# Performance work log

Measured on AMD Instinct MI355X. Metric: run time of the kernel, lower is better.

The kernel has to match this reference:

```python
import jax, jax.numpy as jnp
import numpy as np

B, L, H, E = 4, 2048, 8, 64
S, D = L, E  # causal mask forces L == S


def setup_inputs() -> dict:
    key = jax.random.key(0)
    kq, kk, kv, km = jax.random.split(key, 4)
    return {
        "queries": jax.random.normal(kq, (B, L, H, E), dtype=jnp.float32),
        "keys": jax.random.normal(kk, (B, S, H, E), dtype=jnp.float32),
        "values": jax.random.normal(kv, (B, S, H, D), dtype=jnp.float32),
        "map": jax.random.normal(km, (S, S), dtype=jnp.float32),
    }


def reference(queries, keys, values, map):
    # queries: [B,L,H,E], keys: [B,S,H,E], values: [B,S,H,D], map: [S,S]
    E_ = queries.shape[-1]
    scale = 1.0 / jnp.sqrt(jnp.asarray(E_, dtype=queries.dtype))
    # raw attention scores: [B,H,L,S]
    scores = jnp.einsum("blhe,bshe->bhls", queries, keys)
    # mix scores with learned map along the key axis: [B,H,L,S]
    scores = jnp.einsum("bhls,st->bhlt", scores, map)
    # causal mask (TriangularCausalMask: triu with diagonal=1 is masked)
    Lq = queries.shape[1]
    causal = jnp.triu(jnp.ones((Lq, Lq), dtype=bool), k=1)  # [L,S]
    scores = jnp.where(causal[None, None, :, :], -jnp.inf, scores)
    attn = jax.nn.softmax(scale * scores, axis=-1)  # dropout p=0.0 -> identity
    out = jnp.einsum("bhls,bshd->blhd", attn, values)  # [B,L,H,D]
    return out
```

## Files before the change

kernel.cpp:

```cpp
#include <hip/hip_runtime.h>


typedef short bf16x8 __attribute__((ext_vector_type(8)));
typedef float f32x4 __attribute__((ext_vector_type(4)));
typedef float f32x16 __attribute__((ext_vector_type(16)));
typedef unsigned short u16x8 __attribute__((ext_vector_type(8)));

typedef __attribute__((address_space(1))) const void gvoid;
typedef __attribute__((address_space(3))) void lvoid;

__device__ __forceinline__ unsigned short f2bf(float x) {
  unsigned int u = __float_as_uint(x);
  u += 0x7FFFu + ((u >> 16) & 1u);
  return (unsigned short)(u >> 16);
}
__device__ __forceinline__ float bf2f(unsigned short h) {
  return __uint_as_float(((unsigned int)h) << 16);
}

__device__ __forceinline__ void gload16(const unsigned short* g, unsigned short* l) {
  __builtin_amdgcn_global_load_lds((gvoid*)g, (lvoid*)l, 16, 0, 0);
}

__device__ __forceinline__ void stage_tile(const unsigned short* __restrict__ g,
                                           int gstride, unsigned short* l,
                                           int rows, int tid) {
  const int lane = tid & 63, w = tid >> 6;
  const int nch = rows << 3;
  for (int c0 = (w << 6); c0 < nch; c0 += 256) {
    const int c = c0 + lane;
    const int row = c >> 3;
    const int bir = (c & 7) << 4;
    const int sb = bir ^ ((row & 7) << 4);
    gload16(g + (size_t)row * gstride + (sb >> 1), l + (size_t)c0 * 8);
  }
}

__device__ __forceinline__ int swz(int row, int byteInRow) {
  return row * 128 + (byteInRow ^ ((row & 7) << 4));
}

__global__ __launch_bounds__(256) void prep_m(const float* __restrict__ M,
                                              unsigned short* __restrict__ Mh,
                                              unsigned short* __restrict__ Ml) {
  __shared__ float Ts[64][68];
  const int s0 = blockIdx.x << 6, t0 = blockIdx.y << 6;
  const int tid = threadIdx.x, r = tid >> 2, c0 = (tid & 3) << 4;
  const float* src = M + (size_t)(s0 + r) * 2048 + t0 + c0;
#pragma unroll
  for (int j = 0; j < 4; ++j)
    *(float4*)&Ts[r][c0 + 4 * j] = *(const float4*)(src + 4 * j);
  __syncthreads();
  u16x8 h0, h1, l0v, l1v;
#pragma unroll
  for (int j = 0; j < 8; ++j) {
    float x = Ts[c0 + j][r];
    unsigned short hh = f2bf(x);
    h0[j] = hh; l0v[j] = f2bf(x - bf2f(hh));
  }
#pragma unroll
  for (int j = 8; j < 16; ++j) {
    float x = Ts[c0 + j][r];
    unsigned short hh = f2bf(x);
    h1[j - 8] = hh; l1v[j - 8] = f2bf(x - bf2f(hh));
  }
  const size_t o = (size_t)(t0 + r) * 2048 + s0 + c0;
  *(u16x8*)(Mh + o) = h0; *(u16x8*)(Mh + o + 8) = h1;
  *(u16x8*)(Ml + o) = l0v; *(u16x8*)(Ml + o + 8) = l1v;
}

__global__ __launch_bounds__(256) void prep_kv(const float* __restrict__ src4d,
                                               unsigned short* __restrict__ Dh,
                                               unsigned short* __restrict__ Dl,
                                               int has_lo) {
  __shared__ float Ts[64][68];
  const int s0 = blockIdx.x << 6, bh = blockIdx.y;
  const int b = bh >> 3, h = bh & 7;
  const int tid = threadIdx.x, r = tid >> 2, c0 = (tid & 3) << 4;
  const float* src = src4d + ((size_t)(b * 2048 + s0 + r) * 8 + h) * 64 + c0;
#pragma unroll
  for (int j = 0; j < 4; ++j)
    *(float4*)&Ts[r][c0 + 4 * j] = *(const float4*)(src + 4 * j);
  __syncthreads();
  u16x8 h0, h1, l0v, l1v;
#pragma unroll
  for (int j = 0; j < 8; ++j) {
    float x = Ts[c0 + j][r];
    unsigned short hh = f2bf(x);
    h0[j] = hh; l0v[j] = f2bf(x - bf2f(hh));
  }
#pragma unroll
  for (int j = 8; j < 16; ++j) {
    float x = Ts[c0 + j][r];
    unsigned short hh = f2bf(x);
    h1[j - 8] = hh; l1v[j - 8] = f2bf(x - bf2f(hh));
  }
  const size_t o = ((size_t)bh * 64 + r) * 2048 + s0 + c0;
  *(u16x8*)(Dh + o) = h0; *(u16x8*)(Dh + o + 8) = h1;
  if (has_lo) { *(u16x8*)(Dl + o) = l0v; *(u16x8*)(Dl + o + 8) = l1v; }
}

__global__ __launch_bounds__(256) void km_mfma(
    const unsigned short* __restrict__ Mth, const unsigned short* __restrict__ Mtl,
    const unsigned short* __restrict__ Kth, const unsigned short* __restrict__ Ktl,
    unsigned short* __restrict__ KMh, unsigned short* __restrict__ KMl) {
  __shared__ __attribute__((aligned(16))) unsigned short sm[24576];
  unsigned short* MtH = sm;
  unsigned short* MtL = sm + 8192;
  unsigned short* KtH = sm + 16384;
  unsigned short* KtL = sm + 20480;
  const int tid = threadIdx.x, lane = tid & 63, w = tid >> 6;
  const int g = lane >> 4, li = lane & 15;
  const int t0 = blockIdx.x << 7;
  const int bh = blockIdx.y;
  const unsigned short* KtHb = Kth + (size_t)bh * 64 * 2048;
  const unsigned short* KtLb = Ktl + (size_t)bh * 64 * 2048;

  f32x4 acc[2][4];
#pragma unroll
  for (int mi = 0; mi < 2; ++mi)
#pragma unroll
    for (int ni = 0; ni < 4; ++ni) acc[mi][ni] = (f32x4){0.f, 0.f, 0.f, 0.f};

  for (int s0 = 0; s0 < 2048; s0 += 64) {
    __syncthreads();
    stage_tile(Mth + (size_t)t0 * 2048 + s0, 2048, MtH, 128, tid);
    stage_tile(Mtl + (size_t)t0 * 2048 + s0, 2048, MtL, 128, tid);
    stage_tile(KtHb + s0, 2048, KtH, 64, tid);
    stage_tile(KtLb + s0, 2048, KtL, 64, tid);
    asm volatile("s_waitcnt vmcnt(0)" ::: "memory");
    __syncthreads();
#pragma unroll
    for (int kk = 0; kk < 2; ++kk) {
      const int kb = (kk * 32 + 8 * g) * 2;
      bf16x8 aH[2], aL[2];
#pragma unroll
      for (int mi = 0; mi < 2; ++mi) {
        const int row = (w << 5) + (mi << 4) + li;
        aH[mi] = *(const bf16x8*)((const char*)MtH + swz(row, kb));
        aL[mi] = *(const bf16x8*)((const char*)MtL + swz(row, kb));
      }
#pragma unroll
      for (int ni = 0; ni < 4; ++ni) {
        const int row = (ni << 4) + li;
        const int off = swz(row, kb);
        const bf16x8 bH = *(const bf16x8*)((const char*)KtH + off);
        const bf16x8 bL = *(const bf16x8*)((const char*)KtL + off);
#pragma unroll
        for (int mi = 0; mi < 2; ++mi) {
          acc[mi][ni] = __builtin_amdgcn_mfma_f32_16x16x32_bf16(aH[mi], bH, acc[mi][ni], 0, 0, 0);
          acc[mi][ni] = __builtin_amdgcn_mfma_f32_16x16x32_bf16(aH[mi], bL, acc[mi][ni], 0, 0, 0);
          acc[mi][ni] = __builtin_amdgcn_mfma_f32_16x16x32_bf16(aL[mi], bH, acc[mi][ni], 0, 0, 0);
        }
      }
    }
  }
  const size_t base = (size_t)bh * 2048 * 64;
#pragma unroll
  for (int mi = 0; mi < 2; ++mi)
#pragma unroll
    for (int r = 0; r < 4; ++r) {
      const int trow = t0 + (w << 5) + (mi << 4) + (g << 2) + r;
#pragma unroll
      for (int ni = 0; ni < 4; ++ni) {
        const float x = acc[mi][ni][r];
        const unsigned short hh = f2bf(x);
        const size_t idx = base + (size_t)trow * 64 + (ni << 4) + li;
        KMh[idx] = hh;
        KMl[idx] = f2bf(x - bf2f(hh));
      }
    }
}

__global__ __launch_bounds__(256, 2) void attn32(
    const float* __restrict__ Q, const unsigned short* __restrict__ KMh,
    const unsigned short* __restrict__ KMl, const unsigned short* __restrict__ Vt,
    float* __restrict__ Out) {
  __shared__ __attribute__((aligned(16))) unsigned short sm[32768];
  const int tid = threadIdx.x, lane = tid & 63, w = tid >> 6;
  const int g2 = lane >> 5, li5 = lane & 31;
  unsigned short* PS = sm + 24576 + (w << 11);

  const int bid = (int)blockIdx.x;
  const int x = bid & 7;
  const int r = bid >> 3;
  const int m = r >> 2;
  const int bh = (x << 2) | (r & 3);
  const int lt = (m < 8) ? (15 - m) : (m - 8);
  const int b = bh >> 3, h = bh & 7;
  const int l0 = lt << 7;
  const int qg = l0 + (w << 5) + li5;

  bf16x8 qh[4], ql[4];
  {
    const float* qsrc = Q + (((size_t)(b * 2048 + qg) * 8 + h) << 6) + (g2 << 3);
#pragma unroll
    for (int kk = 0; kk < 4; ++kk) {
      const float4 v0 = *(const float4*)(qsrc + 16 * kk);
      const float4 v1 = *(const float4*)(qsrc + 16 * kk + 4);
      const float xs[8] = {v0.x, v0.y, v0.z, v0.w, v1.x, v1.y, v1.z, v1.w};
#pragma unroll
      for (int j = 0; j < 8; ++j) {
        const unsigned short hh = f2bf(xs[j]);
        qh[kk][j] = (short)hh;
        ql[kk][j] = (short)f2bf(xs[j] - bf2f(hh));
      }
    }
  }

  f32x16 o0 = {0,0,0,0,0,0,0,0,0,0,0,0,0,0,0,0};
  f32x16 o1 = {0,0,0,0,0,0,0,0,0,0,0,0,0,0,0,0};
  float m2 = -1e30f, lsum = 0.f;
  const float SC2 = 0.18033688011112042f;

  const unsigned short* KHb = KMh + (size_t)bh * 2048 * 64;
  const unsigned short* KLb = KMl + (size_t)bh * 2048 * 64;
  const unsigned short* VTb = Vt + (size_t)bh * 64 * 2048;

  const int jtmax_blk = 2 * lt + 1;
  const int jtmax_w = 2 * lt + (w >> 1);

  {
    unsigned short* s0b = sm;
    stage_tile(KHb, 64, s0b, 64, tid);
    stage_tile(KLb, 64, s0b + 4096, 64, tid);
    stage_tile(VTb, 2048, s0b + 8192, 64, tid);
  }
  asm volatile("s_waitcnt vmcnt(0)" ::: "memory");
  __builtin_amdgcn_s_barrier();
  __builtin_amdgcn_sched_barrier(0);

  for (int jt = 0; jt <= jtmax_blk; ++jt) {
    const int cur = jt & 1;
    if (jt < jtmax_blk) {
      unsigned short* nb = sm + (cur ^ 1) * 12288;
      stage_tile(KHb + (size_t)(jt + 1) * 4096, 64, nb, 64, tid);
      stage_tile(KLb + (size_t)(jt + 1) * 4096, 64, nb + 4096, 64, tid);
      stage_tile(VTb + (jt + 1) * 64, 2048, nb + 8192, 64, tid);
    }

    if (jt <= jtmax_w) {
      const unsigned short* KH = sm + cur * 12288;
      const unsigned short* KL = KH + 4096;
      const unsigned short* VT = KH + 8192;

      f32x16 z0 = {0,0,0,0,0,0,0,0,0,0,0,0,0,0,0,0};
      f32x16 z1 = {0,0,0,0,0,0,0,0,0,0,0,0,0,0,0,0};
      __builtin_amdgcn_s_setprio(1);
#pragma unroll
      for (int kk = 0; kk < 4; ++kk) {
        const int cb = 32 * kk + 16 * g2;
        const bf16x8 a0h = *(const bf16x8*)((const char*)KH + swz(li5, cb));
        const bf16x8 a0l = *(const bf16x8*)((const char*)KL + swz(li5, cb));
        const bf16x8 a1h = *(const bf16x8*)((const char*)KH + swz(32 + li5, cb));
        const bf16x8 a1l = *(const bf16x8*)((const char*)KL + swz(32 + li5, cb));
        z0 = __builtin_amdgcn_mfma_f32_32x32x16_bf16(a0h, qh[kk], z0, 0, 0, 0);
        z0 = __builtin_amdgcn_mfma_f32_32x32x16_bf16(a0h, ql[kk], z0, 0, 0, 0);
        z0 = __builtin_amdgcn_mfma_f32_32x32x16_bf16(a0l, qh[kk], z0, 0, 0, 0);
        z1 = __builtin_amdgcn_mfma_f32_32x32x16_bf16(a1h, qh[kk], z1, 0, 0, 0);
        z1 = __builtin_amdgcn_mfma_f32_32x32x16_bf16(a1h, ql[kk], z1, 0, 0, 0);
        z1 = __builtin_amdgcn_mfma_f32_32x32x16_bf16(a1l, qh[kk], z1, 0, 0, 0);
      }
      __builtin_amdgcn_s_setprio(0);

      const bool needmask = (jt * 64 + 63 > l0 + (w << 5));
      const int thr = qg - jt * 64;
      if (needmask) {
#pragma unroll
        for (int rr = 0; rr < 16; ++rr) {
          const int tl = (g2 << 2) + ((rr >> 2) << 3) + (rr & 3);
          z0[rr] = (tl > thr) ? -1e30f : z0[rr] * SC2;
          z1[rr] = (tl + 32 > thr) ? -1e30f : z1[rr] * SC2;
        }
      } else {
#pragma unroll
        for (int rr = 0; rr < 16; ++rr) { z0[rr] *= SC2; z1[rr] *= SC2; }
      }

      float t16[16];
#pragma unroll
      for (int rr = 0; rr < 16; ++rr) t16[rr] = fmaxf(z0[rr], z1[rr]);
#pragma unroll
      for (int s = 8; s; s >>= 1)
#pragma unroll
        for (int rr = 0; rr < 8; ++rr)
          if (rr < s) t16[rr] = fmaxf(t16[rr], t16[rr + s]);
      float mx = fmaxf(t16[0], __shfl_xor(t16[0], 32));
      const float m2n = fmaxf(m2, mx);
      const float fs = exp2f(m2 - m2n);
      m2 = m2n;
      float pv0[16], pv1[16];
#pragma unroll
      for (int rr = 0; rr < 16; ++rr) {
        pv0[rr] = exp2f(z0[rr] - m2n);
        pv1[rr] = exp2f(z1[rr] - m2n);
      }
      float s16[16];
#pragma unroll
      for (int rr = 0; rr < 16; ++rr) s16[rr] = pv0[rr] + pv1[rr];
#pragma unroll
      for (int s = 8; s; s >>= 1)
#pragma unroll
        for (int rr = 0; rr < 8; ++rr)
          if (rr < s) s16[rr] += s16[rr + s];
      float rs = s16[0] + __shfl_xor(s16[0], 32);
      lsum = lsum * fs + rs;
#pragma unroll
      for (int rr = 0; rr < 16; ++rr) { o0[rr] *= fs; o1[rr] *= fs; }

#pragma unroll
      for (int r2 = 0; r2 < 4; ++r2) {
        const int bb = (r2 << 4) + (g2 << 3);
        uint a0 = (uint)f2bf(pv0[4 * r2]) | ((uint)f2bf(pv0[4 * r2 + 1]) << 16);
        uint a1 = (uint)f2bf(pv0[4 * r2 + 2]) | ((uint)f2bf(pv0[4 * r2 + 3]) << 16);
        *(uint2*)((char*)PS + swz(li5, bb)) = make_uint2(a0, a1);
        uint b0 = (uint)f2bf(pv1[4 * r2]) | ((uint)f2bf(pv1[4 * r2 + 1]) << 16);
        uint b1 = (uint)f2bf(pv1[4 * r2 + 2]) | ((uint)f2bf(pv1[4 * r2 + 3]) << 16);
        *(uint2*)((char*)PS + swz(li5, 64 + bb)) = make_uint2(b0, b1);
      }

      __builtin_amdgcn_s_setprio(1);
#pragma unroll
      for (int kk = 0; kk < 4; ++kk) {
        const int cb = 32 * kk + 16 * g2;
        const bf16x8 pf = *(const bf16x8*)((const char*)PS + swz(li5, cb));
        const bf16x8 v0f = *(const bf16x8*)((const char*)VT + swz(li5, cb));
        const bf16x8 v1f = *(const bf16x8*)((const char*)VT + swz(32 + li5, cb));
        o0 = __builtin_amdgcn_mfma_f32_32x32x16_bf16(v0f, pf, o0, 0, 0, 0);
        o1 = __builtin_amdgcn_mfma_f32_32x32x16_bf16(v1f, pf, o1, 0, 0, 0);
      }
      __builtin_amdgcn_s_setprio(0);
    }

    asm volatile("s_waitcnt vmcnt(0)" ::: "memory");
    __builtin_amdgcn_s_barrier();
    __builtin_amdgcn_sched_barrier(0);
  }

  const float inv = 1.f / lsum;
  float* ob = Out + (((size_t)(b * 2048 + qg) * 8 + h) << 6);
#pragma unroll
  for (int r2 = 0; r2 < 4; ++r2) {
    const int doff = (g2 << 2) + (r2 << 3);
    float4 s0 = make_float4(o0[4 * r2] * inv, o0[4 * r2 + 1] * inv,
                            o0[4 * r2 + 2] * inv, o0[4 * r2 + 3] * inv);
    *(float4*)(ob + doff) = s0;
    float4 s1 = make_float4(o1[4 * r2] * inv, o1[4 * r2 + 1] * inv,
                            o1[4 * r2 + 2] * inv, o1[4 * r2 + 3] * inv);
    *(float4*)(ob + 32 + doff) = s1;
  }
}

extern "C" void kernel_launch(void* const* d_in, const int* in_sizes, int n_in,
                              void* d_out, int out_size, void* d_ws, size_t ws_size,
                              hipStream_t stream) {
  const float* Q = (const float*)d_in[0];
  const float* K = (const float*)d_in[1];
  const float* V = (const float*)d_in[2];
  const float* M = (const float*)d_in[3];
  float* Out = (float*)d_out;
  char* ws = (char*)d_ws;
  const size_t MB = 1u << 20;
  unsigned short* Mth = (unsigned short*)(ws);
  unsigned short* Mtl = (unsigned short*)(ws + 8 * MB);
  unsigned short* Kth = (unsigned short*)(ws + 16 * MB);
  unsigned short* Ktl = (unsigned short*)(ws + 24 * MB);
  unsigned short* Vts = (unsigned short*)(ws + 32 * MB);
  unsigned short* KMh = (unsigned short*)(ws + 40 * MB);
  unsigned short* KMl = (unsigned short*)(ws + 48 * MB);

  prep_m<<<dim3(32, 32), 256, 0, stream>>>(M, Mth, Mtl);
  prep_kv<<<dim3(32, 32), 256, 0, stream>>>(K, Kth, Ktl, 1);
  prep_kv<<<dim3(32, 32), 256, 0, stream>>>(V, Vts, (unsigned short*)nullptr, 0);
  km_mfma<<<dim3(16, 32), 256, 0, stream>>>(Mth, Mtl, Kth, Ktl, KMh, KMl);
  attn32<<<dim3(512), 256, 0, stream>>>(Q, KMh, KMl, Vts, Out);
}
```

Measured before the change: 154.8 us.

## Keep P in registers via permlane swap, lazy rescale, MFMA row-sum, prescaled Q

Moves the softmax scale into the Q bf16 split so score tiles no longer need a per-element multiply. P is converted with packed bf16 conversions and rearranged across lane halves with v_permlane32_swap instead of a round trip through shared memory, which lets the shared buffer shrink. The row sum is now computed by an extra MFMA against a ones vector in place of a shuffle reduction. Rescaling of the output and the running max is skipped unless the new max exceeds the old one by a threshold. The price is an extra MFMA per k-step and larger unnormalised exponentials, bounded by the threshold.

```diff
diff --git a/kernel.cpp b/kernel.cpp
--- a/kernel.cpp
+++ b/kernel.cpp
@@ -5,6 +5,7 @@
 typedef float f32x4 __attribute__((ext_vector_type(4)));
 typedef float f32x16 __attribute__((ext_vector_type(16)));
 typedef unsigned short u16x8 __attribute__((ext_vector_type(8)));
+typedef unsigned int u32x4 __attribute__((ext_vector_type(4)));
 
 typedef __attribute__((address_space(1))) const void gvoid;
 typedef __attribute__((address_space(3))) void lvoid;
@@ -16,6 +17,11 @@
 }
 __device__ __forceinline__ float bf2f(unsigned short h) {
   return __uint_as_float(((unsigned int)h) << 16);
+}
+__device__ __forceinline__ unsigned int cvtpk(float lo, float hi) {
+  unsigned int r;
+  asm("v_cvt_pk_bf16_f32 %0, %1, %2" : "=v"(r) : "v"(lo), "v"(hi));
+  return r;
 }
 
 __device__ __forceinline__ void gload16(const unsigned short* g, unsigned short* l) {
@@ -176,10 +182,9 @@
     const float* __restrict__ Q, const unsigned short* __restrict__ KMh,
     const unsigned short* __restrict__ KMl, const unsigned short* __restrict__ Vt,
     float* __restrict__ Out) {
-  __shared__ __attribute__((aligned(16))) unsigned short sm[32768];
+  __shared__ __attribute__((aligned(16))) unsigned short sm[24576];
   const int tid = threadIdx.x, lane = tid & 63, w = tid >> 6;
   const int g2 = lane >> 5, li5 = lane & 31;
-  unsigned short* PS = sm + 24576 + (w << 11);
 
   const int bid = (int)blockIdx.x;
   const int x = bid & 7;
@@ -191,6 +196,7 @@
   const int l0 = lt << 7;
   const int qg = l0 + (w << 5) + li5;
 
+  const float SC2 = 0.18033688011112042f;
   bf16x8 qh[4], ql[4];
   {
     const float* qsrc = Q + (((size_t)(b * 2048 + qg) * 8 + h) << 6) + (g2 << 3);
@@ -201,17 +207,21 @@
       const float xs[8] = {v0.x, v0.y, v0.z, v0.w, v1.x, v1.y, v1.z, v1.w};
 #pragma unroll
       for (int j = 0; j < 8; ++j) {
-        const unsigned short hh = f2bf(xs[j]);
+        const float xv = xs[j] * SC2;
+        const unsigned short hh = f2bf(xv);
         qh[kk][j] = (short)hh;
-        ql[kk][j] = (short)f2bf(xs[j] - bf2f(hh));
+        ql[kk][j] = (short)f2bf(xv - bf2f(hh));
       }
     }
   }
 
   f32x16 o0 = {0,0,0,0,0,0,0,0,0,0,0,0,0,0,0,0};
   f32x16 o1 = {0,0,0,0,0,0,0,0,0,0,0,0,0,0,0,0};
-  float m2 = -1e30f, lsum = 0.f;
-  const float SC2 = 0.18033688011112042f;
+  f32x16 lsacc = {0,0,0,0,0,0,0,0,0,0,0,0,0,0,0,0};
+  float m2 = -1e30f;
+  bf16x8 ones;
+#pragma unroll
+  for (int j = 0; j < 8; ++j) ones[j] = (short)0x3F80;
 
   const unsigned short* KHb = KMh + (size_t)bh * 2048 * 64;
   const unsigned short* KLb = KMl + (size_t)bh * 2048 * 64;
@@ -264,17 +274,14 @@
       __builtin_amdgcn_s_setprio(0);
 
       const bool needmask = (jt * 64 + 63 > l0 + (w << 5));
-      const int thr = qg - jt * 64;
       if (needmask) {
+        const int thr = qg - jt * 64;
 #pragma unroll
         for (int rr = 0; rr < 16; ++rr) {
           const int tl = (g2 << 2) + ((rr >> 2) << 3) + (rr & 3);
-          z0[rr] = (tl > thr) ? -1e30f : z0[rr] * SC2;
-          z1[rr] = (tl + 32 > thr) ? -1e30f : z1[rr] * SC2;
+          if (tl > thr) z0[rr] = -1e30f;
+          if (tl + 32 > thr) z1[rr] = -1e30f;
         }
-      } else {
-#pragma unroll
-        for (int rr = 0; rr < 16; ++rr) { z0[rr] *= SC2; z1[rr] *= SC2; }
       }
 
       float t16[16];
@@ -285,49 +292,57 @@
 #pragma unroll
         for (int rr = 0; rr < 8; ++rr)
           if (rr < s) t16[rr] = fmaxf(t16[rr], t16[rr + s]);
-      float mx = fmaxf(t16[0], __shfl_xor(t16[0], 32));
-      const float m2n = fmaxf(m2, mx);
-      const float fs = exp2f(m2 - m2n);
-      m2 = m2n;
+      const float mx = fmaxf(t16[0], __shfl_xor(t16[0], 32));
+      if (__any(mx > m2 + 11.0f)) {
+        const float m2n = fmaxf(m2, mx);
+        const float fs = exp2f(m2 - m2n);
+        m2 = m2n;
+#pragma unroll
+        for (int rr = 0; rr < 16; ++rr) { o0[rr] *= fs; o1[rr] *= fs; }
+        lsacc[0] *= fs;
+      }
+
       float pv0[16], pv1[16];
 #pragma unroll
       for (int rr = 0; rr < 16; ++rr) {
-        pv0[rr] = exp2f(z0[rr] - m2n);
-        pv1[rr] = exp2f(z1[rr] - m2n);
-      }
-      float s16[16];
-#pragma unroll
-      for (int rr = 0; rr < 16; ++rr) s16[rr] = pv0[rr] + pv1[rr];
-#pragma unroll
-      for (int s = 8; s; s >>= 1)
-#pragma unroll
-        for (int rr = 0; rr < 8; ++rr)
-          if (rr < s) s16[rr] += s16[rr + s];
-      float rs = s16[0] + __shfl_xor(s16[0], 32);
-      lsum = lsum * fs + rs;
-#pragma unroll
-      for (int rr = 0; rr < 16; ++rr) { o0[rr] *= fs; o1[rr] *= fs; }
-
-#pragma unroll
-      for (int r2 = 0; r2 < 4; ++r2) {
-        const int bb = (r2 << 4) + (g2 << 3);
-        uint a0 = (uint)f2bf(pv0[4 * r2]) | ((uint)f2bf(pv0[4 * r2 + 1]) << 16);
-        uint a1 = (uint)f2bf(pv0[4 * r2 + 2]) | ((uint)f2bf(pv0[4 * r2 + 3]) << 16);
-        *(uint2*)((char*)PS + swz(li5, bb)) = make_uint2(a0, a1);
-        uint b0 = (uint)f2bf(pv1[4 * r2]) | ((uint)f2bf(pv1[4 * r2 + 1]) << 16);
-        uint b1 = (uint)f2bf(pv1[4 * r2 + 2]) | ((uint)f2bf(pv1[4 * r2 + 3]) << 16);
-        *(uint2*)((char*)PS + swz(li5, 64 + bb)) = make_uint2(b0, b1);
+        pv0[rr] = exp2f(z0[rr] - m2);
+        pv1[rr] = exp2f(z1[rr] - m2);
+      }
+      unsigned int W0[8], W1[8];
+#pragma unroll
+      for (int i = 0; i < 8; ++i) {
+        W0[i] = cvtpk(pv0[2 * i], pv0[2 * i + 1]);
+        W1[i] = cvtpk(pv1[2 * i], pv1[2 * i + 1]);
+      }
+      asm volatile("v_permlane32_swap_b32 %0, %1" : "+v"(W0[0]), "+v"(W0[2]));
+      asm volatile("v_permlane32_swap_b32 %0, %1" : "+v"(W0[1]), "+v"(W0[3]));
+      asm volatile("v_permlane32_swap_b32 %0, %1" : "+v"(W0[4]), "+v"(W0[6]));
+      asm volatile("v_permlane32_swap_b32 %0, %1" : "+v"(W0[5]), "+v"(W0[7]));
+      asm volatile("v_permlane32_swap_b32 %0, %1" : "+v"(W1[0]), "+v"(W1[2]));
+      asm volatile("v_permlane32_swap_b32 %0, %1" : "+v"(W1[1]), "+v"(W1[3]));
+      asm volatile("v_permlane32_swap_b32 %0, %1" : "+v"(W1[4]), "+v"(W1[6]));
+      asm volatile("v_permlane32_swap_b32 %0, %1" : "+v"(W1[5]), "+v"(W1[7]));
+      bf16x8 pf[4];
+      {
+        u32x4 f0 = {W0[0], W0[1], W0[2], W0[3]};
+        u32x4 f1 = {W0[4], W0[5], W0[6], W0[7]};
+        u32x4 f2 = {W1[0], W1[1], W1[2], W1[3]};
+        u32x4 f3 = {W1[4], W1[5], W1[6], W1[7]};
+        pf[0] = __builtin_bit_cast(bf16x8, f0);
+        pf[1] = __builtin_bit_cast(bf16x8, f1);
+        pf[2] = __builtin_bit_cast(bf16x8, f2);
+        pf[3] = __builtin_bit_cast(bf16x8, f3);
       }
 
       __builtin_amdgcn_s_setprio(1);
 #pragma unroll
       for (int kk = 0; kk < 4; ++kk) {
         const int cb = 32 * kk + 16 * g2;
-        const bf16x8 pf = *(const bf16x8*)((const char*)PS + swz(li5, cb));
         const bf16x8 v0f = *(const bf16x8*)((const char*)VT + swz(li5, cb));
         const bf16x8 v1f = *(const bf16x8*)((const char*)VT + swz(32 + li5, cb));
-        o0 = __builtin_amdgcn_mfma_f32_32x32x16_bf16(v0f, pf, o0, 0, 0, 0);
-        o1 = __builtin_amdgcn_mfma_f32_32x32x16_bf16(v1f, pf, o1, 0, 0, 0);
+        o0 = __builtin_amdgcn_mfma_f32_32x32x16_bf16(v0f, pf[kk], o0, 0, 0, 0);
+        o1 = __builtin_amdgcn_mfma_f32_32x32x16_bf16(v1f, pf[kk], o1, 0, 0, 0);
+        lsacc = __builtin_amdgcn_mfma_f32_32x32x16_bf16(ones, pf[kk], lsacc, 0, 0, 0);
       }
       __builtin_amdgcn_s_setprio(0);
     }
@@ -337,7 +352,7 @@
     __builtin_amdgcn_sched_barrier(0);
   }
 
-  const float inv = 1.f / lsum;
+  const float inv = 1.f / lsacc[0];
   float* ob = Out + (((size_t)(b * 2048 + qg) * 8 + h) << 6);
 #pragma unroll
   for (int r2 = 0; r2 < 4; ++r2) {
```

After: 147.5 us. 4.7% less time.
